# Kernel tuning notes

Measured on AMD Instinct MI355X. Metric: run time of the kernel, lower is better.

Reference implementation:

```python
import jax, jax.numpy as jnp
import numpy as np

P = 16          # patch size
D = 256         # embed dim (complex channels)
L = 2           # depth (num blocks)
NE = 4          # num experts
FF = 1024       # ffn hidden = expand * D
B, T, C, IH, IW = 1, 8, 4, 256, 256
HP, WP = IH // P, IW // P


def setup_inputs():
    key = jax.random.key(0)
    ks = iter(jax.random.split(key, 40))
    r = lambda shape, s=0.02: jax.random.normal(next(ks), shape, jnp.float32) * s
    sD = 1.0 / np.sqrt(D)
    return {
        'x': jax.random.normal(next(ks), (B, T, C, IH, IW), jnp.float32),
        'dt': jax.random.uniform(next(ks), (B, T), jnp.float32, 0.1, 1.0),
        'Wenc': r((C * P * P, 2 * D)),
        'benc': jnp.zeros((2 * D,), jnp.float32),
        'Wdec': r((2 * D, C * P * P)),
        'bdec': jnp.zeros((C * P * P,), jnp.float32),
        'ln_sp_w': jnp.ones((L, 2 * D), jnp.float32),
        'ln_sp_b': jnp.zeros((L, 2 * D), jnp.float32),
        'conv_w': r((L, 2 * D, 2 * D, 3, 3)),
        'conv_b': jnp.zeros((L, 2 * D), jnp.float32),
        'E_re': r((L, D, D), sD), 'E_im': r((L, D, D), sD),
        'Ed_re': r((L, D, D), sD), 'Ed_im': r((L, D, D), sD),
        'Ws_re': r((L, D, D), sD), 'Ws_im': r((L, D, D), sD),
        'Wg': r((L, 2 * D, D)),
        'bg': jnp.zeros((L, D), jnp.float32),
        'lam_re': r((L, D), 1.0), 'lam_im': r((L, D), 1.0),
        'ln_t_w': jnp.ones((L, 2 * D), jnp.float32),
        'ln_t_b': jnp.zeros((L, 2 * D), jnp.float32),
        'Wr': r((L, 2 * D, NE)),
        'W1': r((L, NE, 2 * D, FF)),
        'W2': r((L, NE, FF, 2 * D)),
    }


def _ln(x, w, b):
    m = x.mean(-1, keepdims=True)
    v = ((x - m) ** 2).mean(-1, keepdims=True)
    return (x - m) * jax.lax.rsqrt(v + 1e-5) * w + b


def _block(z, h_prev, flux_prev, dt, bp):
    (ln_sp_w, ln_sp_b, conv_w, conv_b, E_re, E_im, Ed_re, Ed_im,
     Ws_re, Ws_im, Wg, bg, lam_re, lam_im, ln_t_w, ln_t_b, Wr, W1, W2) = bp
    Bq, Tq, Dq, H, W = z.shape
    # --- spatial process: LN + conv on concat(real, imag), complex residual ---
    zf = z.reshape(Bq * Tq, Dq, H, W)
    zr = jnp.concatenate([zf.real, zf.imag], axis=1)
    zn = _ln(zr.transpose(0, 2, 3, 1), ln_sp_w, ln_sp_b).transpose(0, 3, 1, 2)
    zs = jax.lax.conv_general_dilated(zn, conv_w, (1, 1), 'SAME',
                                      dimension_numbers=('NCHW', 'OIHW', 'NCHW'))
    zs = zs + conv_b[None, :, None, None]
    re, im = jnp.split(zs, 2, axis=1)
    x = (zf + (re + 1j * im)).reshape(Bq, Tq, Dq, H, W)
    # --- eigen-basis encode ---
    Eb = E_re + 1j * E_im
    x_eigen = jnp.einsum('btdhw,de->bthwe', x, Eb)   # [B,T,H,W,D] complex
    x_mean = x_eigen.mean(axis=(2, 3))               # [B,T,D] complex
    # --- sequential gated flux recurrence over T ---
    Ws = Ws_re + 1j * Ws_im
    def step(flux, xm):
        source = xm @ Ws
        feat = jnp.concatenate([xm.real, xm.imag], -1)
        gate = jax.nn.sigmoid(feat @ Wg + bg)        # real [B,D]
        new_flux = gate * flux + (1.0 - gate) * source
        return new_flux, (new_flux, source, gate)
    _, (flux_seq, source_seq, gate_seq) = jax.lax.scan(step, flux_prev, x_mean.transpose(1, 0, 2))
    flux_seq = flux_seq.transpose(1, 0, 2)
    source_seq = source_seq.transpose(1, 0, 2)
    gate_seq = gate_seq.transpose(1, 0, 2)
    g = gate_seq[:, :, None, None, :]
    forcing = x_eigen * g + source_seq[:, :, None, None, :] * (1.0 - g)
    # --- transition operators ---
    lam = -(jax.nn.softplus(lam_re) + 1e-2) + 1j * lam_im        # [D]
    op_decay = jnp.exp(lam[None, None, :] * dt[:, :, None])      # [B,T,D] complex
    op_forcing = (op_decay - 1.0) / lam
    a = jnp.broadcast_to(op_decay[:, :, None, None, :], forcing.shape)
    u = forcing * op_forcing[:, :, None, None, :]
    # --- parallel linear scan h_t = a_t * h_{t-1} + u_t along T ---
    def comb(c1, c2):
        a1, u1 = c1
        a2, u2 = c2
        return a1 * a2, u1 * a2 + u2
    _, h = jax.lax.associative_scan(comb, (a, u), axis=1)
    # as written in source: h_prev contribution is h_prev * op_decay at every t
    h = h + h_prev.reshape(Bq, 1, H, W, Dq) * a
    last_h = h[:, -1].reshape(Bq * H * W, 1, Dq)
    last_flux = flux_seq[:, -1]
    # --- eigen decode + temporal LN + MoE FFN ---
    Ed = Ed_re + 1j * Ed_im
    x_out = jnp.einsum('bthwe,ed->btdhw', h, Ed)
    xf = x_out.reshape(Bq * Tq, Dq, H, W)
    xr = jnp.concatenate([xf.real, xf.imag], axis=1)
    xn = _ln(xr.transpose(0, 2, 3, 1), ln_t_w, ln_t_b)           # [BT,H,W,2D]
    tok = xn.reshape(-1, 2 * Dq)
    probs = jax.nn.softmax(tok @ Wr, axis=-1)                    # [N,E]
    hid = jax.nn.gelu(jnp.einsum('nd,edf->nef', tok, W1))
    y = jnp.einsum('nef,efd,ne->nd', hid, W2, probs)             # [N,2D]
    xc = xn[..., :Dq] + 1j * xn[..., Dq:]
    delta = (y[..., :Dq] + 1j * y[..., Dq:]).reshape(Bq * Tq, H, W, Dq)
    x_cplx = (xc + delta).reshape(Bq, Tq, H, W, Dq).transpose(0, 1, 4, 2, 3)
    return x + x_cplx, last_h, last_flux


def _forward(x, dt, Wenc, benc, Wdec, bdec, ln_sp_w, ln_sp_b, conv_w, conv_b,
             E_re, E_im, Ed_re, Ed_im, Ws_re, Ws_im, Wg, bg, lam_re, lam_im,
             ln_t_w, ln_t_b, Wr, W1, W2):
    # encoder: patchify + linear -> complex latent [B,T,D,HP,WP]
    xp = x.reshape(B, T, C, HP, P, WP, P).transpose(0, 1, 3, 5, 2, 4, 6)
    xp = xp.reshape(B, T, HP, WP, C * P * P)
    ze = xp @ Wenc + benc                                        # [B,T,HP,WP,2D]
    z = (ze[..., :D] + 1j * ze[..., D:]).transpose(0, 1, 4, 2, 3)
    h_prev = jnp.zeros((B * HP * WP, 1, D), jnp.complex64)
    flux_prev = jnp.zeros((B, D), jnp.complex64)
    bparams = (ln_sp_w, ln_sp_b, conv_w, conv_b, E_re, E_im, Ed_re, Ed_im,
               Ws_re, Ws_im, Wg, bg, lam_re, lam_im, ln_t_w, ln_t_b, Wr, W1, W2)
    for i in range(L):
        bp = tuple(p[i] for p in bparams)
        z, h_prev, flux_prev = _block(z, h_prev, flux_prev, dt, bp)
    # decoder: linear + unpatchify (real output)
    zr = jnp.concatenate([z.real, z.imag], axis=2).transpose(0, 1, 3, 4, 2)
    yo = zr @ Wdec + bdec                                        # [B,T,HP,WP,C*P*P]
    out = yo.reshape(B, T, HP, WP, C, P, P).transpose(0, 1, 4, 2, 5, 3, 6)
    return out.reshape(B, T, C, IH, IW)


def reference(x, dt, Wenc, benc, Wdec, bdec, ln_sp_w, ln_sp_b, conv_w, conv_b,
              E_re, E_im, Ed_re, Ed_im, Ws_re, Ws_im, Wg, bg, lam_re, lam_im,
              ln_t_w, ln_t_b, Wr, W1, W2):
    return _forward(x, dt, Wenc, benc, Wdec, bdec, ln_sp_w, ln_sp_b, conv_w, conv_b,
                    E_re, E_im, Ed_re, Ed_im, Ws_re, Ws_im, Wg, bg, lam_re, lam_im,
                    ln_t_w, ln_t_b, Wr, W1, W2)
```

## Files before the change

### kernel.cpp

```cpp
#include <hip/hip_runtime.h>
#include <hip/hip_bf16.h>


#define TOKS 2048
#define PSLICE 1048576

typedef __bf16 bf16;
typedef __attribute__((ext_vector_type(8))) __bf16 bf16x8;
typedef __attribute__((ext_vector_type(4))) __bf16 bf16x4;
typedef __attribute__((ext_vector_type(4))) float f32x4;

enum GMode { EENC = 0, ECONV, ESQ, EMOE1, EMOE2, EDEC };

template <int MODE, int SPLIT>
__global__ __launch_bounds__(256) void mgemm_k(
    const bf16* __restrict__ A, const bf16* __restrict__ Bt,
    const float* __restrict__ bias, const float* __restrict__ scalev,
    float* __restrict__ C, bf16* __restrict__ C16, float* __restrict__ Cpart,
    int K, int N) {
  __shared__ __align__(16) bf16 As[64 * 40];
  __shared__ __align__(16) bf16 Bs[64 * 40];
  const int tid = threadIdx.x;
  const int bm = blockIdx.x * 64, bn = blockIdx.y * 64;
  const int lane = tid & 63, w = tid >> 6;
  const int wm = (w & 1) * 32, wn = (w >> 1) * 32;
  const int quad = lane >> 4, l16 = lane & 15;
  const int srow = tid >> 2, sko = (tid & 3) << 3;

  const int kbase = (SPLIT > 1) ? blockIdx.z * (K / SPLIT) : 0;
  const int kiter = K / (32 * SPLIT);
  if constexpr (MODE == EMOE1) Bt += (size_t)blockIdx.z * 524288;

  f32x4 acc[2][2] = {};

  int cv_t = 0, cv_h = 0, cv_w = 0;
  if constexpr (MODE == ECONV) {
    const int gm = bm + srow;
    cv_t = gm >> 8;
    cv_h = (gm >> 4) & 15;
    cv_w = gm & 15;
  }

  auto loadA = [&](int kt) -> bf16x8 {
    const int gk = kbase + kt * 32 + sko;
    if constexpr (MODE == ECONV) {
      const int s = gk >> 9, ci = gk & 511;
      const int kh = s / 3, kw = s - kh * 3;
      const int hh = cv_h + kh - 1, ww = cv_w + kw - 1;
      if (hh >= 0 && hh < 16 && ww >= 0 && ww < 16)
        return *(const bf16x8*)&A[(size_t)(((cv_t << 8) + hh * 16 + ww) << 9) +
                                  ci];
      bf16x8 zz;
#pragma unroll
      for (int q = 0; q < 8; q++) zz[q] = (bf16)0.0f;
      return zz;
    } else {
      return *(const bf16x8*)&A[(size_t)(bm + srow) * K + gk];
    }
  };
  auto loadB = [&](int kt) -> bf16x8 {
    return *(const bf16x8*)&Bt[(size_t)(bn + srow) * K + kbase + kt * 32 + sko];
  };

  bf16x8 pa = loadA(0), pb = loadB(0);
  for (int kt = 0; kt < kiter; kt++) {
    *(bf16x8*)&As[srow * 40 + sko] = pa;
    *(bf16x8*)&Bs[srow * 40 + sko] = pb;
    __syncthreads();
    if (kt + 1 < kiter) {
      pa = loadA(kt + 1);
      pb = loadB(kt + 1);
    }
    const bf16x8 a0 = *(const bf16x8*)&As[(wm + l16) * 40 + quad * 8];
    const bf16x8 a1 = *(const bf16x8*)&As[(wm + 16 + l16) * 40 + quad * 8];
    const bf16x8 b0 = *(const bf16x8*)&Bs[(wn + l16) * 40 + quad * 8];
    const bf16x8 b1 = *(const bf16x8*)&Bs[(wn + 16 + l16) * 40 + quad * 8];
    acc[0][0] = __builtin_amdgcn_mfma_f32_16x16x32_bf16(a0, b0, acc[0][0], 0, 0, 0);
    acc[0][1] = __builtin_amdgcn_mfma_f32_16x16x32_bf16(a0, b1, acc[0][1], 0, 0, 0);
    acc[1][0] = __builtin_amdgcn_mfma_f32_16x16x32_bf16(a1, b0, acc[1][0], 0, 0, 0);
    acc[1][1] = __builtin_amdgcn_mfma_f32_16x16x32_bf16(a1, b1, acc[1][1], 0, 0, 0);
    __syncthreads();
  }

#pragma unroll
  for (int i = 0; i < 2; i++) {
#pragma unroll
    for (int j = 0; j < 2; j++) {
#pragma unroll
      for (int r = 0; r < 4; r++) {
        const int gm = bm + wm + i * 16 + quad * 4 + r;
        const int gn = bn + wn + j * 16 + l16;
        const float v = acc[i][j][r];
        if constexpr (SPLIT > 1) {
          Cpart[(size_t)blockIdx.z * PSLICE + (size_t)gm * 512 + gn] = v;
        } else if constexpr (MODE == EMOE1) {
          const float t = 0.7978845608028654f * (v + 0.044715f * v * v * v);
          const float g = 0.5f * v * (1.f + tanhf(t));
          const float p = scalev[gm * 4 + blockIdx.z];
          C16[(size_t)gm * 4096 + blockIdx.z * 1024 + gn] = (bf16)(p * g);
        } else {
          const int t = gm >> 8, hp = (gm >> 4) & 15, wp = gm & 15;
          const int c = gn >> 8, ph = (gn >> 4) & 15, pw = gn & 15;
          C[(size_t)(((t * 4 + c) * 256 + hp * 16 + ph) << 8) + wp * 16 + pw] =
              v + bias[gn];
        }
      }
    }
  }
}

__global__ __launch_bounds__(256) void conv_ep_k(
    const float* __restrict__ parts, const float* __restrict__ bias,
    const float* __restrict__ resid, float* __restrict__ xb,
    bf16* __restrict__ xb16) {
  const int i4 = (blockIdx.x * 256 + threadIdx.x) << 2;
  const int c = i4 & 511;
  const float4 p0 = *(const float4*)&parts[i4];
  const float4 p1 = *(const float4*)&parts[PSLICE + i4];
  const float4 p2 = *(const float4*)&parts[2 * PSLICE + i4];
  const float4 p3 = *(const float4*)&parts[3 * PSLICE + i4];
  const float4 bi = *(const float4*)&bias[c];
  const float4 rz = *(const float4*)&resid[i4];
  float4 o;
  o.x = p0.x + p1.x + p2.x + p3.x + bi.x + rz.x;
  o.y = p0.y + p1.y + p2.y + p3.y + bi.y + rz.y;
  o.z = p0.z + p1.z + p2.z + p3.z + bi.z + rz.z;
  o.w = p0.w + p1.w + p2.w + p3.w + bi.w + rz.w;
  *(float4*)&xb[i4] = o;
  bf16x4 o16 = {(bf16)o.x, (bf16)o.y, (bf16)o.z, (bf16)o.w};
  *(bf16x4*)&xb16[i4] = o16;
}

template <bool ENC>
__global__ __launch_bounds__(256) void ln_comb_k(
    const float* __restrict__ parts, const float* __restrict__ bias,
    const float* __restrict__ w, const float* __restrict__ b,
    const float* __restrict__ Wr, float* __restrict__ zout,
    float* __restrict__ out32, bf16* __restrict__ out16,
    float* __restrict__ probs) {
  const int wv = threadIdx.x >> 6, lane = threadIdx.x & 63;
  const int n = (blockIdx.x << 2) + wv;
  float v[8];
  float s = 0.f, s2 = 0.f;
#pragma unroll
  for (int i = 0; i < 8; i++) {
    const int c = (i << 6) + lane;
    float x = parts[(size_t)n * 512 + c] + parts[PSLICE + (size_t)n * 512 + c];
    if constexpr (ENC) x += bias[c];
    v[i] = x;
    s += x;
    s2 += x * x;
  }
#pragma unroll
  for (int off = 32; off > 0; off >>= 1) {
    s += __shfl_down(s, off);
    s2 += __shfl_down(s2, off);
  }
  s = __shfl(s, 0);
  s2 = __shfl(s2, 0);
  const float m = s * (1.f / 512.f);
  const float var = s2 * (1.f / 512.f) - m * m;
  const float r = rsqrtf(var + 1e-5f);
  float a0 = 0.f, a1 = 0.f, a2 = 0.f, a3 = 0.f;
#pragma unroll
  for (int i = 0; i < 8; i++) {
    const int c = (i << 6) + lane;
    const float o = (v[i] - m) * r * w[c] + b[c];
    if constexpr (ENC) {
      zout[(size_t)n * 512 + c] = v[i];
    } else {
      out32[(size_t)n * 512 + c] = o;
      a0 += o * Wr[c * 4 + 0];
      a1 += o * Wr[c * 4 + 1];
      a2 += o * Wr[c * 4 + 2];
      a3 += o * Wr[c * 4 + 3];
    }
    out16[(size_t)n * 512 + c] = (bf16)o;
  }
  if constexpr (!ENC) {
#pragma unroll
    for (int off = 32; off > 0; off >>= 1) {
      a0 += __shfl_down(a0, off);
      a1 += __shfl_down(a1, off);
      a2 += __shfl_down(a2, off);
      a3 += __shfl_down(a3, off);
    }
    if (lane == 0) {
      const float mx = fmaxf(fmaxf(a0, a1), fmaxf(a2, a3));
      const float e0 = expf(a0 - mx), e1 = expf(a1 - mx), e2 = expf(a2 - mx),
                  e3 = expf(a3 - mx);
      const float inv = 1.f / (e0 + e1 + e2 + e3);
      probs[n * 4 + 0] = e0 * inv;
      probs[n * 4 + 1] = e1 * inv;
      probs[n * 4 + 2] = e2 * inv;
      probs[n * 4 + 3] = e3 * inv;
    }
  }
}

template <bool DO_LN>
__global__ __launch_bounds__(256) void addf2_k(
    const float* __restrict__ xb, const float* __restrict__ xn,
    const float* __restrict__ parts, const float* __restrict__ w,
    const float* __restrict__ b, float* __restrict__ zout,
    bf16* __restrict__ out16) {
  const int wv = threadIdx.x >> 6, lane = threadIdx.x & 63;
  const int n = (blockIdx.x << 2) + wv;
  float v[8];
  float s = 0.f, s2 = 0.f;
#pragma unroll
  for (int i = 0; i < 8; i++) {
    const size_t idx = (size_t)n * 512 + (i << 6) + lane;
    const float x = xb[idx] + xn[idx] + parts[idx] + parts[PSLICE + idx] +
                    parts[2 * PSLICE + idx] + parts[3 * PSLICE + idx];
    v[i] = x;
    s += x;
    s2 += x * x;
  }
  if constexpr (!DO_LN) {
#pragma unroll
    for (int i = 0; i < 8; i++)
      out16[(size_t)n * 512 + (i << 6) + lane] = (bf16)v[i];
    return;
  }
#pragma unroll
  for (int off = 32; off > 0; off >>= 1) {
    s += __shfl_down(s, off);
    s2 += __shfl_down(s2, off);
  }
  s = __shfl(s, 0);
  s2 = __shfl(s2, 0);
  const float m = s * (1.f / 512.f);
  const float var = s2 * (1.f / 512.f) - m * m;
  const float r = rsqrtf(var + 1e-5f);
#pragma unroll
  for (int i = 0; i < 8; i++) {
    const int c = (i << 6) + lane;
    const float x = v[i];
    zout[(size_t)n * 512 + c] = x;
    out16[(size_t)n * 512 + c] = (bf16)((x - m) * r * w[c] + b[c]);
  }
}

__global__ __launch_bounds__(256) void cvt_all_k(
    const float* __restrict__ x, const float* __restrict__ Wenc,
    const float* __restrict__ Wdec, const float* __restrict__ W1,
    const float* __restrict__ W2, const float* __restrict__ E_re,
    const float* __restrict__ E_im, const float* __restrict__ Ed_re,
    const float* __restrict__ Ed_im, const float* __restrict__ conv_w,
    bf16* __restrict__ Ae, bf16* __restrict__ WencT, bf16* __restrict__ WdecT,
    bf16* __restrict__ W1T, bf16* __restrict__ W2Tc, bf16* __restrict__ MEt,
    bf16* __restrict__ convBt) {
  __shared__ float smem[4608];
  float(*tile)[33] = (float(*)[33])smem;
  const int tid = threadIdx.x;
  int b = blockIdx.x;
  const int tx = tid & 31, ty = tid >> 5;
  auto tpose = [&](const float* src, bf16* dst, int N, int dstride, int k0,
                   int n0) {
#pragma unroll
    for (int r = 0; r < 4; r++)
      tile[ty + 8 * r][tx] = src[(size_t)(k0 + ty + 8 * r) * N + n0 + tx];
    __syncthreads();
#pragma unroll
    for (int r = 0; r < 4; r++)
      dst[(size_t)(n0 + ty + 8 * r) * dstride + k0 + tx] =
          (bf16)tile[tx][ty + 8 * r];
  };
  if (b < 1024) {
    const int id = b * 256 + tid;
    const int n = id >> 7;
    const int kc = (id & 127) << 3;
    const int t = n >> 8, hp = (n >> 4) & 15, wp = n & 15;
    const int c = kc >> 8, ph = (kc >> 4) & 15, pw = kc & 15;
    const float* src =
        &x[(size_t)(((t * 4 + c) * 256 + hp * 16 + ph) << 8) + wp * 16 + pw];
    const float4 v0 = *(const float4*)src;
    const float4 v1 = *(const float4*)(src + 4);
    bf16* d = &Ae[(size_t)n * 1024 + kc];
    d[0] = (bf16)v0.x; d[1] = (bf16)v0.y; d[2] = (bf16)v0.z; d[3] = (bf16)v0.w;
    d[4] = (bf16)v1.x; d[5] = (bf16)v1.y; d[6] = (bf16)v1.z; d[7] = (bf16)v1.w;
    return;
  }
  b -= 1024;
  if (b < 512) {
    tpose(Wenc, WencT, 512, 1024, (b & 31) * 32, (b >> 5) * 32);
    return;
  }
  b -= 512;
  if (b < 512) {
    tpose(Wdec, WdecT, 1024, 512, (b & 15) * 32, (b >> 4) * 32);
    return;
  }
  b -= 512;
  if (b < 4096) {
    const int z = b >> 9, rem = b & 511;
    tpose(W1 + (size_t)z * 524288, W1T + (size_t)z * 524288, 1024, 512,
          (rem & 15) * 32, (rem >> 4) * 32);
    return;
  }
  b -= 4096;
  if (b < 4096) {
    const int z = b >> 9, rem = b & 511;
    const int l = z >> 2, e = z & 3;
    tpose(W2 + (size_t)z * 524288, W2Tc + (size_t)l * 2097152 + e * 1024, 512,
          4096, (rem & 31) * 32, (rem >> 5) * 32);
    return;
  }
  b -= 4096;
  if (b < 4096) {
    const int z = b >> 10;
    const int l = z >> 1, which = z & 1;
    const float* Er = (which ? Ed_re : E_re) + l * 65536;
    const float* Ei = (which ? Ed_im : E_im) + l * 65536;
    bf16* dst = MEt + (size_t)z * 262144;
    const int idx = (b & 1023) * 256 + tid;
    const int j = idx >> 9, k = idx & 511;
    const int kk = k & 255, jj = j & 255;
    const float er = Er[kk * 256 + jj], ei = Ei[kk * 256 + jj];
    const float v = (k < 256) ? ((j < 256) ? er : ei) : ((j < 256) ? -ei : er);
    dst[idx] = (bf16)v;
    return;
  }
  b -= 4096;
  {
    const int l = b >> 9, co = b & 511;
    const float* src = conv_w + (size_t)l * 2359296 + (size_t)co * 4608;
    bf16* d = convBt + (size_t)l * 2359296 + (size_t)co * 4608;
    for (int i = tid; i < 4608; i += 256) smem[i] = src[i];
    __syncthreads();
    for (int o = tid; o < 4608; o += 256) {
      const int s = o >> 9, ci = o & 511;
      d[o] = (bf16)smem[ci * 9 + s];
    }
  }
}

__global__ __launch_bounds__(256) void srcgate_k(
    const float* __restrict__ parts, const float* __restrict__ Wsr,
    const float* __restrict__ Wsi, const float* __restrict__ Wg,
    const float* __restrict__ bg, float* __restrict__ srcs,
    float* __restrict__ gts) {
  const int t = blockIdx.x, part = blockIdx.y, d = threadIdx.x;
  __shared__ float sxm[512];
  for (int c = d; c < 512; c += 256) {
    const float* col0 = parts + (size_t)(t << 8) * 512 + c;
    const float* col1 = col0 + PSLICE;
    float s0 = 0.f, s1 = 0.f;
    for (int p = 0; p < 256; p += 2) {
      s0 += col0[(size_t)p * 512] + col1[(size_t)p * 512];
      s1 += col0[(size_t)(p + 1) * 512] + col1[(size_t)(p + 1) * 512];
    }
    sxm[c] = (s0 + s1) * (1.f / 256.f);
  }
  __syncthreads();
  if (part == 0) {
    float s0 = 0.f, s1 = 0.f, s2 = 0.f, s3 = 0.f;
#pragma unroll 4
    for (int e = 0; e < 256; e += 4) {
      s0 += sxm[e + 0] * Wsr[(e + 0) * 256 + d] - sxm[256 + e + 0] * Wsi[(e + 0) * 256 + d];
      s1 += sxm[e + 1] * Wsr[(e + 1) * 256 + d] - sxm[256 + e + 1] * Wsi[(e + 1) * 256 + d];
      s2 += sxm[e + 2] * Wsr[(e + 2) * 256 + d] - sxm[256 + e + 2] * Wsi[(e + 2) * 256 + d];
      s3 += sxm[e + 3] * Wsr[(e + 3) * 256 + d] - sxm[256 + e + 3] * Wsi[(e + 3) * 256 + d];
    }
    srcs[t * 512 + d] = (s0 + s1) + (s2 + s3);
  } else if (part == 1) {
    float s0 = 0.f, s1 = 0.f, s2 = 0.f, s3 = 0.f;
#pragma unroll 4
    for (int e = 0; e < 256; e += 4) {
      s0 += sxm[e + 0] * Wsi[(e + 0) * 256 + d] + sxm[256 + e + 0] * Wsr[(e + 0) * 256 + d];
      s1 += sxm[e + 1] * Wsi[(e + 1) * 256 + d] + sxm[256 + e + 1] * Wsr[(e + 1) * 256 + d];
      s2 += sxm[e + 2] * Wsi[(e + 2) * 256 + d] + sxm[256 + e + 2] * Wsr[(e + 2) * 256 + d];
      s3 += sxm[e + 3] * Wsi[(e + 3) * 256 + d] + sxm[256 + e + 3] * Wsr[(e + 3) * 256 + d];
    }
    srcs[t * 512 + 256 + d] = (s0 + s1) + (s2 + s3);
  } else {
    float s0 = 0.f, s1 = 0.f, s2 = 0.f, s3 = 0.f;
#pragma unroll 4
    for (int c = 0; c < 512; c += 4) {
      s0 += sxm[c + 0] * Wg[(c + 0) * 256 + d];
      s1 += sxm[c + 1] * Wg[(c + 1) * 256 + d];
      s2 += sxm[c + 2] * Wg[(c + 2) * 256 + d];
      s3 += sxm[c + 3] * Wg[(c + 3) * 256 + d];
    }
    const float ga = (s0 + s1) + (s2 + s3) + bg[d];
    gts[t * 256 + d] = 1.f / (1.f + expf(-ga));
  }
}

template <bool FIRST>
__global__ __launch_bounds__(256) void time_scan_k(
    const float* __restrict__ parts, const float* __restrict__ gts,
    const float* __restrict__ srcs, const float* __restrict__ lamre,
    const float* __restrict__ lamim, const float* __restrict__ dt,
    bf16* __restrict__ hout16, float* __restrict__ hprev) {
  const int d = threadIdx.x;
  const int p = blockIdx.x;
  const float lr0 = lamre[d];
  const float sp = (lr0 > 20.f) ? lr0 : log1pf(expf(lr0));
  const float lre = -(sp + 0.01f);
  const float lim = lamim[d];
  const float den = lre * lre + lim * lim;
  float ar[8], ai[8], ofr[8], ofi[8];
#pragma unroll
  for (int t = 0; t < 8; t++) {
    const float dtv = dt[t];
    const float er = expf(lre * dtv);
    const float odr = er * cosf(lim * dtv);
    const float odi = er * sinf(lim * dtv);
    ar[t] = odr;
    ai[t] = odi;
    const float nr = odr - 1.f, ni = odi;
    ofr[t] = (nr * lre + ni * lim) / den;
    ofi[t] = (ni * lre - nr * lim) / den;
  }
  float hr = 0.f, hi = 0.f;
  float hpr = 0.f, hpi = 0.f;
  if constexpr (!FIRST) {
    hpr = hprev[p * 512 + d];
    hpi = hprev[p * 512 + 256 + d];
  }
  float o7r = 0.f, o7i = 0.f;
#pragma unroll
  for (int t = 0; t < 8; t++) {
    const size_t base = (size_t)((t << 8) + p) * 512;
    const float xr = parts[base + d] + parts[PSLICE + base + d];
    const float xi = parts[base + 256 + d] + parts[PSLICE + base + 256 + d];
    const float g = gts[t * 256 + d];
    const float sr = srcs[t * 512 + d], si = srcs[t * 512 + 256 + d];
    const float fr = xr * g + sr * (1.f - g);
    const float fi = xi * g + si * (1.f - g);
    const float ur = fr * ofr[t] - fi * ofi[t];
    const float ui = fr * ofi[t] + fi * ofr[t];
    const float nhr = ur + ar[t] * hr - ai[t] * hi;
    const float nhi = ui + ar[t] * hi + ai[t] * hr;
    hr = nhr;
    hi = nhi;
    const float outr = hr + ar[t] * hpr - ai[t] * hpi;
    const float outi = hi + ar[t] * hpi + ai[t] * hpr;
    hout16[base + d] = (bf16)outr;
    hout16[base + 256 + d] = (bf16)outi;
    if (t == 7) {
      o7r = outr;
      o7i = outi;
    }
  }
  hprev[p * 512 + d] = o7r;
  hprev[p * 512 + 256 + d] = o7i;
}

extern "C" void kernel_launch(void* const* d_in, const int* in_sizes, int n_in,
                              void* d_out, int out_size, void* d_ws,
                              size_t ws_size, hipStream_t stream) {
  const float* x_in = (const float*)d_in[0];
  const float* dt = (const float*)d_in[1];
  const float* Wenc = (const float*)d_in[2];
  const float* benc = (const float*)d_in[3];
  const float* Wdec = (const float*)d_in[4];
  const float* bdec = (const float*)d_in[5];
  const float* ln_sp_w = (const float*)d_in[6];
  const float* ln_sp_b = (const float*)d_in[7];
  const float* conv_w = (const float*)d_in[8];
  const float* conv_b = (const float*)d_in[9];
  const float* E_re = (const float*)d_in[10];
  const float* E_im = (const float*)d_in[11];
  const float* Ed_re = (const float*)d_in[12];
  const float* Ed_im = (const float*)d_in[13];
  const float* Ws_re = (const float*)d_in[14];
  const float* Ws_im = (const float*)d_in[15];
  const float* Wg = (const float*)d_in[16];
  const float* bg = (const float*)d_in[17];
  const float* lam_re = (const float*)d_in[18];
  const float* lam_im = (const float*)d_in[19];
  const float* ln_t_w = (const float*)d_in[20];
  const float* ln_t_b = (const float*)d_in[21];
  const float* Wr = (const float*)d_in[22];
  const float* W1 = (const float*)d_in[23];
  const float* W2 = (const float*)d_in[24];
  float* out = (float*)d_out;

  float* ws = (float*)d_ws;
  size_t off = 0;
  auto allocf = [&](size_t n) {
    float* p = ws + off;
    off += n;
    return p;
  };
  auto allocb = [&](size_t n) {
    bf16* p = (bf16*)(ws + off);
    off += n / 2;
    return p;
  };
  float* z = allocf((size_t)TOKS * 512);
  float* xn = allocf((size_t)TOKS * 512);
  float* xb = allocf((size_t)TOKS * 512);
  float* parts = allocf((size_t)4 * PSLICE);
  float* hprev = allocf(256 * 512);
  float* srcs = allocf(8 * 512);
  float* gts = allocf(8 * 256);
  float* probs = allocf((size_t)TOKS * 4);
  bf16* znsp16 = allocb((size_t)TOKS * 512);
  bf16* xn16 = allocb((size_t)TOKS * 512);
  bf16* xb16 = allocb((size_t)TOKS * 512);
  bf16* z16 = allocb((size_t)TOKS * 512);
  bf16* hb16 = allocb((size_t)TOKS * 512);
  bf16* hid16 = allocb((size_t)TOKS * 4096);
  bf16* Aenc16 = allocb((size_t)TOKS * 1024);
  bf16* WencT = allocb((size_t)512 * 1024);
  bf16* WdecT = allocb((size_t)1024 * 512);
  bf16* MEt = allocb((size_t)4 * 512 * 512);
  bf16* convBt = allocb((size_t)2 * 512 * 4608);
  bf16* W1T = allocb((size_t)8 * 1024 * 512);
  bf16* W2Tc = allocb((size_t)2 * 512 * 4096);

  cvt_all_k<<<15360, 256, 0, stream>>>(x_in, Wenc, Wdec, W1, W2, E_re, E_im,
                                       Ed_re, Ed_im, conv_w, Aenc16, WencT,
                                       WdecT, W1T, W2Tc, MEt, convBt);

  mgemm_k<EENC, 2><<<dim3(32, 8, 2), 256, 0, stream>>>(
      Aenc16, WencT, nullptr, nullptr, nullptr, nullptr, parts, 1024, 512);
  ln_comb_k<true><<<512, 256, 0, stream>>>(parts, benc, ln_sp_w, ln_sp_b,
                                           nullptr, z, nullptr, znsp16,
                                           nullptr);

  for (int l = 0; l < 2; l++) {
    mgemm_k<ECONV, 4><<<dim3(32, 8, 4), 256, 0, stream>>>(
        znsp16, convBt + (size_t)l * 2359296, nullptr, nullptr, nullptr,
        nullptr, parts, 4608, 512);
    conv_ep_k<<<1024, 256, 0, stream>>>(parts, conv_b + l * 512, z, xb, xb16);
    mgemm_k<ESQ, 2><<<dim3(32, 8, 2), 256, 0, stream>>>(
        xb16, MEt + (size_t)(l * 2) * 262144, nullptr, nullptr, nullptr,
        nullptr, parts, 512, 512);
    srcgate_k<<<dim3(8, 3), 256, 0, stream>>>(parts, Ws_re + l * 65536,
                                              Ws_im + l * 65536,
                                              Wg + l * 131072, bg + l * 256,
                                              srcs, gts);
    if (l == 0)
      time_scan_k<true><<<256, 256, 0, stream>>>(parts, gts, srcs, lam_re,
                                                 lam_im, dt, hb16, hprev);
    else
      time_scan_k<false><<<256, 256, 0, stream>>>(parts, gts, srcs,
                                                  lam_re + 256, lam_im + 256,
                                                  dt, hb16, hprev);
    mgemm_k<ESQ, 2><<<dim3(32, 8, 2), 256, 0, stream>>>(
        hb16, MEt + (size_t)(l * 2 + 1) * 262144, nullptr, nullptr, nullptr,
        nullptr, parts, 512, 512);
    ln_comb_k<false><<<512, 256, 0, stream>>>(parts, nullptr, ln_t_w + l * 512,
                                              ln_t_b + l * 512, Wr + l * 2048,
                                              nullptr, xn, xn16, probs);
    mgemm_k<EMOE1, 1><<<dim3(32, 16, 4), 256, 0, stream>>>(
        xn16, W1T + (size_t)l * 2097152, nullptr, probs, nullptr, hid16,
        nullptr, 512, 1024);
    mgemm_k<EMOE2, 4><<<dim3(32, 8, 4), 256, 0, stream>>>(
        hid16, W2Tc + (size_t)l * 2097152, nullptr, nullptr, nullptr, nullptr,
        parts, 4096, 512);
    if (l == 0)
      addf2_k<true><<<512, 256, 0, stream>>>(xb, xn, parts, ln_sp_w + 512,
                                             ln_sp_b + 512, z, znsp16);
    else
      addf2_k<false><<<512, 256, 0, stream>>>(xb, xn, parts, nullptr, nullptr,
                                              nullptr, z16);
  }

  mgemm_k<EDEC, 1><<<dim3(32, 16), 256, 0, stream>>>(
      z16, WdecT, bdec, nullptr, out, nullptr, nullptr, 512, 1024);
}
```

Before: 478.5 us.

## Raise split-K to 8 for conv/MoE2 GEMMs and fuse token-mean into GEMM epilogue

Doubles the split-K factor of the conv and second MoE GEMMs from 4 to 8, launching twice as many workgroups so the 256-CU device is better filled, and extends the reduction kernels to sum eight partial slices. Separately, the first square GEMM now accumulates per-time-step column sums into a small buffer with atomics, so the source/gate kernel no longer rereads the full partial buffers to compute means. The cost is more partial-buffer traffic (8 slices written and read) and atomic contention plus float-order nondeterminism in the mean.

After: 458.8 us. 1.04x faster.

```diff
diff --git a/kernel.cpp b/kernel.cpp
--- a/kernel.cpp
+++ b/kernel.cpp
@@ -10,14 +10,14 @@
 typedef __attribute__((ext_vector_type(4))) __bf16 bf16x4;
 typedef __attribute__((ext_vector_type(4))) float f32x4;
 
-enum GMode { EENC = 0, ECONV, ESQ, EMOE1, EMOE2, EDEC };
+enum GMode { EENC = 0, ECONV, ESQ, ESQM, EMOE1, EMOE2, EDEC };
 
 template <int MODE, int SPLIT>
 __global__ __launch_bounds__(256) void mgemm_k(
     const bf16* __restrict__ A, const bf16* __restrict__ Bt,
     const float* __restrict__ bias, const float* __restrict__ scalev,
     float* __restrict__ C, bf16* __restrict__ C16, float* __restrict__ Cpart,
-    int K, int N) {
+    float* __restrict__ xmean, int K, int N) {
   __shared__ __align__(16) bf16 As[64 * 40];
   __shared__ __align__(16) bf16 Bs[64 * 40];
   const int tid = threadIdx.x;
@@ -107,25 +107,35 @@
       }
     }
   }
+  if constexpr (MODE == ESQM) {
+    const int t = bm >> 8;
+#pragma unroll
+    for (int j = 0; j < 2; j++) {
+      float cs = 0.f;
+#pragma unroll
+      for (int i = 0; i < 2; i++)
+#pragma unroll
+        for (int r = 0; r < 4; r++) cs += acc[i][j][r];
+      atomicAdd(&xmean[t * 512 + bn + wn + j * 16 + l16], cs);
+    }
+  }
 }
 
 __global__ __launch_bounds__(256) void conv_ep_k(
     const float* __restrict__ parts, const float* __restrict__ bias,
     const float* __restrict__ resid, float* __restrict__ xb,
-    bf16* __restrict__ xb16) {
+    bf16* __restrict__ xb16, float* __restrict__ xmean) {
+  if (blockIdx.x < 16) xmean[blockIdx.x * 256 + threadIdx.x] = 0.f;
   const int i4 = (blockIdx.x * 256 + threadIdx.x) << 2;
   const int c = i4 & 511;
-  const float4 p0 = *(const float4*)&parts[i4];
-  const float4 p1 = *(const float4*)&parts[PSLICE + i4];
-  const float4 p2 = *(const float4*)&parts[2 * PSLICE + i4];
-  const float4 p3 = *(const float4*)&parts[3 * PSLICE + i4];
+  float4 o = *(const float4*)&resid[i4];
   const float4 bi = *(const float4*)&bias[c];
-  const float4 rz = *(const float4*)&resid[i4];
-  float4 o;
-  o.x = p0.x + p1.x + p2.x + p3.x + bi.x + rz.x;
-  o.y = p0.y + p1.y + p2.y + p3.y + bi.y + rz.y;
-  o.z = p0.z + p1.z + p2.z + p3.z + bi.z + rz.z;
-  o.w = p0.w + p1.w + p2.w + p3.w + bi.w + rz.w;
+  o.x += bi.x; o.y += bi.y; o.z += bi.z; o.w += bi.w;
+#pragma unroll
+  for (int s = 0; s < 8; s++) {
+    const float4 p = *(const float4*)&parts[(size_t)s * PSLICE + i4];
+    o.x += p.x; o.y += p.y; o.z += p.z; o.w += p.w;
+  }
   *(float4*)&xb[i4] = o;
   bf16x4 o16 = {(bf16)o.x, (bf16)o.y, (bf16)o.z, (bf16)o.w};
   *(bf16x4*)&xb16[i4] = o16;
@@ -211,8 +221,9 @@
 #pragma unroll
   for (int i = 0; i < 8; i++) {
     const size_t idx = (size_t)n * 512 + (i << 6) + lane;
-    const float x = xb[idx] + xn[idx] + parts[idx] + parts[PSLICE + idx] +
-                    parts[2 * PSLICE + idx] + parts[3 * PSLICE + idx];
+    float x = xb[idx] + xn[idx];
+#pragma unroll
+    for (int sl = 0; sl < 8; sl++) x += parts[(size_t)sl * PSLICE + idx];
     v[i] = x;
     s += x;
     s2 += x * x;
@@ -337,22 +348,13 @@
 }
 
 __global__ __launch_bounds__(256) void srcgate_k(
-    const float* __restrict__ parts, const float* __restrict__ Wsr,
+    const float* __restrict__ xmean, const float* __restrict__ Wsr,
     const float* __restrict__ Wsi, const float* __restrict__ Wg,
     const float* __restrict__ bg, float* __restrict__ srcs,
     float* __restrict__ gts) {
   const int t = blockIdx.x, part = blockIdx.y, d = threadIdx.x;
   __shared__ float sxm[512];
-  for (int c = d; c < 512; c += 256) {
-    const float* col0 = parts + (size_t)(t << 8) * 512 + c;
-    const float* col1 = col0 + PSLICE;
-    float s0 = 0.f, s1 = 0.f;
-    for (int p = 0; p < 256; p += 2) {
-      s0 += col0[(size_t)p * 512] + col1[(size_t)p * 512];
-      s1 += col0[(size_t)(p + 1) * 512] + col1[(size_t)(p + 1) * 512];
-    }
-    sxm[c] = (s0 + s1) * (1.f / 256.f);
-  }
+  for (int c = d; c < 512; c += 256) sxm[c] = xmean[t * 512 + c] * (1.f / 256.f);
   __syncthreads();
   if (part == 0) {
     float s0 = 0.f, s1 = 0.f, s2 = 0.f, s3 = 0.f;
@@ -494,8 +496,9 @@
   float* z = allocf((size_t)TOKS * 512);
   float* xn = allocf((size_t)TOKS * 512);
   float* xb = allocf((size_t)TOKS * 512);
-  float* parts = allocf((size_t)4 * PSLICE);
+  float* parts = allocf((size_t)8 * PSLICE);
   float* hprev = allocf(256 * 512);
+  float* xm = allocf(8 * 512);
   float* srcs = allocf(8 * 512);
   float* gts = allocf(8 * 256);
   float* probs = allocf((size_t)TOKS * 4);
@@ -518,20 +521,22 @@
                                        WdecT, W1T, W2Tc, MEt, convBt);
 
   mgemm_k<EENC, 2><<<dim3(32, 8, 2), 256, 0, stream>>>(
-      Aenc16, WencT, nullptr, nullptr, nullptr, nullptr, parts, 1024, 512);
+      Aenc16, WencT, nullptr, nullptr, nullptr, nullptr, parts, nullptr, 1024,
+      512);
   ln_comb_k<true><<<512, 256, 0, stream>>>(parts, benc, ln_sp_w, ln_sp_b,
                                            nullptr, z, nullptr, znsp16,
                                            nullptr);
 
   for (int l = 0; l < 2; l++) {
-    mgemm_k<ECONV, 4><<<dim3(32, 8, 4), 256, 0, stream>>>(
+    mgemm_k<ECONV, 8><<<dim3(32, 8, 8), 256, 0, stream>>>(
         znsp16, convBt + (size_t)l * 2359296, nullptr, nullptr, nullptr,
-        nullptr, parts, 4608, 512);
-    conv_ep_k<<<1024, 256, 0, stream>>>(parts, conv_b + l * 512, z, xb, xb16);
-    mgemm_k<ESQ, 2><<<dim3(32, 8, 2), 256, 0, stream>>>(
+        nullptr, parts, nullptr, 4608, 512);
+    conv_ep_k<<<1024, 256, 0, stream>>>(parts, conv_b + l * 512, z, xb, xb16,
+                                        xm);
+    mgemm_k<ESQM, 2><<<dim3(32, 8, 2), 256, 0, stream>>>(
         xb16, MEt + (size_t)(l * 2) * 262144, nullptr, nullptr, nullptr,
-        nullptr, parts, 512, 512);
-    srcgate_k<<<dim3(8, 3), 256, 0, stream>>>(parts, Ws_re + l * 65536,
+        nullptr, parts, xm, 512, 512);
+    srcgate_k<<<dim3(8, 3), 256, 0, stream>>>(xm, Ws_re + l * 65536,
                                               Ws_im + l * 65536,
                                               Wg + l * 131072, bg + l * 256,
                                               srcs, gts);
@@ -544,16 +549,16 @@
                                                   dt, hb16, hprev);
     mgemm_k<ESQ, 2><<<dim3(32, 8, 2), 256, 0, stream>>>(
         hb16, MEt + (size_t)(l * 2 + 1) * 262144, nullptr, nullptr, nullptr,
-        nullptr, parts, 512, 512);
+        nullptr, parts, nullptr, 512, 512);
     ln_comb_k<false><<<512, 256, 0, stream>>>(parts, nullptr, ln_t_w + l * 512,
                                               ln_t_b + l * 512, Wr + l * 2048,
                                               nullptr, xn, xn16, probs);
     mgemm_k<EMOE1, 1><<<dim3(32, 16, 4), 256, 0, stream>>>(
         xn16, W1T + (size_t)l * 2097152, nullptr, probs, nullptr, hid16,
-        nullptr, 512, 1024);
-    mgemm_k<EMOE2, 4><<<dim3(32, 8, 4), 256, 0, stream>>>(
+        nullptr, nullptr, 512, 1024);
+    mgemm_k<EMOE2, 8><<<dim3(32, 8, 8), 256, 0, stream>>>(
         hid16, W2Tc + (size_t)l * 2097152, nullptr, nullptr, nullptr, nullptr,
-        parts, 4096, 512);
+        parts, nullptr, 4096, 512);
     if (l == 0)
       addf2_k<true><<<512, 256, 0, stream>>>(xb, xn, parts, ln_sp_w + 512,
                                              ln_sp_b + 512, z, znsp16);
@@ -563,5 +568,5 @@
   }
 
   mgemm_k<EDEC, 1><<<dim3(32, 16), 256, 0, stream>>>(
-      z16, WdecT, bdec, nullptr, out, nullptr, nullptr, 512, 1024);
-}
+      z16, WdecT, bdec, nullptr, out, nullptr, nullptr, nullptr, 512, 1024);
+}
```
